# Optimization experiments

Hardware: AMD Instinct MI355X
Metric: run time of the kernel (lower is better)

Reference implementation:

```python
import jax, jax.numpy as jnp
import numpy as np

WS = (2, 7, 7)          # window size (s, h, w)
DIM = 192
HEADS = 6
HEAD_DIM = DIM // HEADS
N = WS[0] * WS[1] * WS[2]  # 98
TABLE = (2 * WS[0] - 1) * (2 * WS[1] - 1) * (2 * WS[2] - 1)  # 507


def _relative_position_index():
    coords = np.stack(np.meshgrid(np.arange(WS[0]), np.arange(WS[1]), np.arange(WS[2]), indexing='ij'))
    cf = coords.reshape(3, -1)                      # [3, N]
    rel = cf[:, :, None] - cf[:, None, :]           # [3, N, N]
    rel = rel.transpose(1, 2, 0).astype(np.int64)   # [N, N, 3]
    rel[..., 0] += WS[0] - 1
    rel[..., 1] += WS[1] - 1
    rel[..., 2] += WS[2] - 1
    rel[..., 0] *= 3 * WS[1] - 1  # faithful to source (quirky multiplier)
    rel[..., 1] *= 2 * WS[1] - 1
    return jnp.asarray(rel.sum(-1), dtype=jnp.int32)  # [N, N]


def setup_inputs() -> dict:
    key = jax.random.key(0)
    ks = jax.random.split(key, 8)
    B_ = 1024
    nW = 64
    skip = jax.random.normal(ks[0], (B_, N, DIM), dtype=jnp.float32)
    x_up = jax.random.normal(ks[1], (B_, N, DIM), dtype=jnp.float32)
    mask = jax.random.normal(ks[2], (nW, N, N), dtype=jnp.float32)
    kv_w = jax.random.normal(ks[3], (DIM, 2 * DIM), dtype=jnp.float32) * 0.02
    kv_b = jnp.zeros((2 * DIM,), dtype=jnp.float32)
    proj_w = jax.random.normal(ks[4], (DIM, DIM), dtype=jnp.float32) * 0.02
    proj_b = jnp.zeros((DIM,), dtype=jnp.float32)
    rpb_table = jax.random.normal(ks[5], (TABLE, HEADS), dtype=jnp.float32) * 0.02
    rel_idx = _relative_position_index()
    return {"skip": skip, "x_up": x_up, "mask": mask, "kv_w": kv_w, "kv_b": kv_b,
            "proj_w": proj_w, "proj_b": proj_b, "rpb_table": rpb_table, "rel_idx": rel_idx}


def reference(skip, x_up, mask, kv_w, kv_b, proj_w, proj_b, rpb_table, rel_idx):
    B_, n, C = skip.shape
    nW = mask.shape[0]
    scale = HEAD_DIM ** -0.5
    kv = skip @ kv_w + kv_b                                # [B_, N, 2C]
    kv = kv.reshape(B_, n, 2, HEADS, HEAD_DIM)
    k = kv[:, :, 0]                                        # [B_, N, H, hd]
    v = kv[:, :, 1]
    q = x_up.reshape(B_, n, HEADS, HEAD_DIM) * scale
    attn = jnp.einsum('bqhd,bkhd->bhqk', q, k)             # [B_, H, N, N]
    bias = rpb_table[rel_idx]                              # [N, N, H]
    attn = attn + jnp.transpose(bias, (2, 0, 1))[None]
    attn = attn.reshape(B_ // nW, nW, HEADS, n, n) + mask[None, :, None]
    attn = attn.reshape(B_, HEADS, n, n)
    attn = jax.nn.softmax(attn, axis=-1)
    out = jnp.einsum('bhqk,bkhd->bqhd', attn, v).reshape(B_, n, C)
    return out @ proj_w + proj_b
```

## Files before the change

### kernel.cpp

```cpp
#include <hip/hip_runtime.h>

#define NTOK 98
#define DIM 192
#define HEADS 6
#define SCALE 0.17677669529663687f

using shortx8 = __attribute__((ext_vector_type(8))) short;
using floatx4 = __attribute__((ext_vector_type(4))) float;

static __device__ __forceinline__ unsigned short f2bf(float f) {
    unsigned u = __float_as_uint(f);
    u += 0x7FFFu + ((u >> 16) & 1u);
    return (unsigned short)(u >> 16);
}

static __device__ __forceinline__ shortx8 pack8(const float* p, float scale) {
    float4 a = *(const float4*)p;
    float4 b = *(const float4*)(p + 4);
    shortx8 t;
    t[0] = (short)f2bf(a.x * scale); t[1] = (short)f2bf(a.y * scale);
    t[2] = (short)f2bf(a.z * scale); t[3] = (short)f2bf(a.w * scale);
    t[4] = (short)f2bf(b.x * scale); t[5] = (short)f2bf(b.y * scale);
    t[6] = (short)f2bf(b.z * scale); t[7] = (short)f2bf(b.w * scale);
    return t;
}

static __device__ __forceinline__ shortx8 frag_from_words(unsigned w0, unsigned w1,
                                                          unsigned w2, unsigned w3) {
    union { unsigned u[4]; shortx8 s; } t;
    t.u[0] = w0; t.u[1] = w1; t.u[2] = w2; t.u[3] = w3;
    return t.s;
}

template <bool HI>
static __device__ __forceinline__ shortx8 xchg4(unsigned lo0, unsigned lo1,
                                                unsigned hi0, unsigned hi1,
                                                int A0b, int A1b, bool hiSel) {
    unsigned l0 = (unsigned)__builtin_amdgcn_ds_bpermute(A0b, (int)lo0);
    unsigned l1 = (unsigned)__builtin_amdgcn_ds_bpermute(A0b, (int)lo1);
    unsigned l2 = (unsigned)__builtin_amdgcn_ds_bpermute(A1b, (int)lo0);
    unsigned l3 = (unsigned)__builtin_amdgcn_ds_bpermute(A1b, (int)lo1);
    unsigned h0 = 0, h1 = 0, h2 = 0, h3 = 0;
    if (HI) {
        h0 = (unsigned)__builtin_amdgcn_ds_bpermute(A0b, (int)hi0);
        h1 = (unsigned)__builtin_amdgcn_ds_bpermute(A0b, (int)hi1);
        h2 = (unsigned)__builtin_amdgcn_ds_bpermute(A1b, (int)hi0);
        h3 = (unsigned)__builtin_amdgcn_ds_bpermute(A1b, (int)hi1);
    }
    return frag_from_words(hiSel ? h0 : l0, hiSel ? h1 : l1,
                           hiSel ? h2 : l2, hiSel ? h3 : l3);
}

__global__ void prep_kernel(const float* __restrict__ rpb, const int* __restrict__ relidx,
                            const float* __restrict__ mask,
                            const float* __restrict__ kvw, const float* __restrict__ pw,
                            float* __restrict__ biasT, float* __restrict__ maskT,
                            unsigned short* __restrict__ kvB, unsigned short* __restrict__ pB) {
    int e = blockIdx.x * 256 + threadIdx.x;
    if (e < HEADS * NTOK * NTOK) {
        int h = e / (NTOK * NTOK), rem = e % (NTOK * NTOK);
        int j = rem / NTOK, i = rem % NTOK;
        biasT[e] = rpb[relidx[i * NTOK + j] * HEADS + h];
    }
    if (e < 64 * NTOK * NTOK) {
        int wd = e / (NTOK * NTOK), rem = e % (NTOK * NTOK);
        int j = rem / NTOK, i = rem % NTOK;
        maskT[e] = mask[((size_t)wd * NTOK + i) * NTOK + j];
    }
    if (e < 73728) {
        int jj = e & 7, lane = (e >> 3) & 63, t = e >> 9;
        int NT = t % 24, ks = t / 24;
        int c = ks * 32 + (lane >> 4) * 8 + jj;
        int n = NT * 16 + (lane & 15);
        kvB[e] = f2bf(kvw[c * 384 + n]);
    }
    if (e < 36864) {
        int jj = e & 7, lane = (e >> 3) & 63, t = e >> 9;
        int NT = t % 12, ks = t / 12;
        int c = ks * 32 + (lane >> 4) * 8 + jj;
        int n = NT * 16 + (lane & 15);
        pB[e] = f2bf(pw[c * 192 + n]);
    }
}

__global__ __launch_bounds__(448, 2) void attn_kernel(
    const float* __restrict__ skip, const float* __restrict__ xup,
    const float* __restrict__ kv_b,
    const float* __restrict__ biasT, const float* __restrict__ maskT,
    const unsigned short* __restrict__ kvB,
    float* __restrict__ out) {

    __shared__ __align__(16) unsigned short kB3[3 * 7 * 512];
    __shared__ __align__(16) unsigned short vB3[3 * 2 * 4 * 512];

    const int tid  = threadIdx.x;
    const int w    = tid >> 6;
    const int lane = tid & 63;
    const int l15  = lane & 15;
    const int quad = lane >> 4;
    const int win  = blockIdx.x >> 1;
    const int g    = blockIdx.x & 1;

    for (int e = tid; e < 6 * 512; e += 448)
        vB3[(e / 512) * 2048 + 3 * 512 + (e & 511)] = 0;
    __syncthreads();

    const int mA  = w * 16 + l15;
    const int mAc = mA < NTOK ? mA : 97;

    const int A0b = ((32 * (quad & 1) + l15) << 2);
    const int A1b = A0b + 64;

    {
        shortx8 afr[6];
        const float* sr = skip + ((size_t)win * NTOK + mAc) * DIM + quad * 8;
        #pragma unroll
        for (int ks = 0; ks < 6; ++ks) afr[ks] = pack8(sr + ks * 32, 1.0f);
        #pragma unroll
        for (int nt = 0; nt < 12; ++nt) {
            const int NTg = (nt < 6) ? (6 * g + nt) : (6 + 6 * g + nt);
            const float cb = kv_b[NTg * 16 + l15];
            floatx4 acc = {cb, cb, cb, cb};
            #pragma unroll
            for (int ks = 0; ks < 6; ++ks) {
                shortx8 bf = *(const shortx8*)(kvB + ((size_t)((ks * 24 + NTg) * 64 + lane)) * 8);
                acc = __builtin_amdgcn_mfma_f32_16x16x32_bf16(afr[ks], bf, acc, 0, 0, 0);
            }
            if (nt < 6) {
                const int ch = nt * 16 + l15, hh = ch >> 5, dh = ch & 31;
                const int base = ((hh * 7 + w) * 64) * 8 + (dh & 7);
                const int lphi = ((dh >> 3) & 3) << 4;
                #pragma unroll
                for (int r = 0; r < 4; ++r) {
                    int mm = quad * 4 + r;
                    kB3[base + (mm | lphi) * 8] = f2bf(acc[r]);
                }
            } else {
                const int cv = (nt - 6) * 16 + l15, hh = cv >> 5, dh = cv & 31, ntv = dh >> 4;
                #pragma unroll
                for (int r = 0; r < 4; ++r) {
                    int m = w * 16 + quad * 4 + r;
                    if (m < NTOK) {
                        int lp = (dh & 15) | (((m >> 3) & 3) << 4);
                        vB3[(((hh * 2 + ntv) * 4 + (m >> 5)) * 64 + lp) * 8 + (m & 7)] = f2bf(acc[r]);
                    }
                }
            }
        }
    }
    __syncthreads();

    #pragma unroll
    for (int hp = 0; hp < 3; ++hp) {
        const int h = 3 * g + hp;
        shortx8 qf = pack8(xup + ((size_t)win * NTOK + mAc) * DIM + h * 32 + quad * 8, SCALE);

        floatx4 S[7];
        {
            const float* bT = biasT + (size_t)h * (NTOK * NTOK);
            const float* mT = maskT + (size_t)(win & 63) * (NTOK * NTOK);
            #pragma unroll
            for (int nt = 0; nt < 7; ++nt) {
                #pragma unroll
                for (int r = 0; r < 4; ++r) {
                    int j = nt * 16 + quad * 4 + r;
                    S[nt][r] = (j < NTOK) ? (bT[j * NTOK + mAc] + mT[j * NTOK + mAc])
                                          : -1e30f;
                }
            }
        }
        #pragma unroll
        for (int nt = 0; nt < 7; ++nt) {
            shortx8 bk = *(const shortx8*)&kB3[((hp * 7 + nt) * 64 + lane) * 8];
            S[nt] = __builtin_amdgcn_mfma_f32_16x16x32_bf16(bk, qf, S[nt], 0, 0, 0);
        }
        float mx;
        {
            float m0 = fmaxf(fmaxf(S[0][0], S[0][1]), fmaxf(S[0][2], S[0][3]));
            float m1 = fmaxf(fmaxf(S[1][0], S[1][1]), fmaxf(S[1][2], S[1][3]));
            float m2 = fmaxf(fmaxf(S[2][0], S[2][1]), fmaxf(S[2][2], S[2][3]));
            float m3 = fmaxf(fmaxf(S[3][0], S[3][1]), fmaxf(S[3][2], S[3][3]));
            float m4 = fmaxf(fmaxf(S[4][0], S[4][1]), fmaxf(S[4][2], S[4][3]));
            float m5 = fmaxf(fmaxf(S[5][0], S[5][1]), fmaxf(S[5][2], S[5][3]));
            float m6 = fmaxf(fmaxf(S[6][0], S[6][1]), fmaxf(S[6][2], S[6][3]));
            mx = fmaxf(fmaxf(fmaxf(m0, m1), fmaxf(m2, m3)), fmaxf(fmaxf(m4, m5), m6));
            mx = fmaxf(mx, __shfl_xor(mx, 16));
            mx = fmaxf(mx, __shfl_xor(mx, 32));
        }
        float sm = 0.f;
        #pragma unroll
        for (int nt = 0; nt < 7; ++nt) {
            #pragma unroll
            for (int r = 0; r < 4; ++r) { S[nt][r] = __expf(S[nt][r] - mx); }
            sm += (S[nt][0] + S[nt][1]) + (S[nt][2] + S[nt][3]);
        }
        sm += __shfl_xor(sm, 16);
        sm += __shfl_xor(sm, 32);
        const float inv = 1.0f / sm;

        unsigned pk[7][2];
        #pragma unroll
        for (int nt = 0; nt < 7; ++nt) {
            pk[nt][0] = (unsigned)f2bf(S[nt][0]) | ((unsigned)f2bf(S[nt][1]) << 16);
            pk[nt][1] = (unsigned)f2bf(S[nt][2]) | ((unsigned)f2bf(S[nt][3]) << 16);
        }
        floatx4 o0 = {0.f, 0.f, 0.f, 0.f}, o1 = {0.f, 0.f, 0.f, 0.f};
        const bool hiSel = (quad & 2) != 0;
        #pragma unroll
        for (int ks = 0; ks < 4; ++ks) {
            shortx8 pfr;
            if (ks < 3)
                pfr = xchg4<true>(pk[2 * ks][0], pk[2 * ks][1],
                                  pk[2 * ks + 1][0], pk[2 * ks + 1][1], A0b, A1b, hiSel);
            else
                pfr = xchg4<false>(pk[6][0], pk[6][1], 0u, 0u, A0b, A1b, hiSel);
            shortx8 vb0 = *(const shortx8*)&vB3[(((hp * 2 + 0) * 4 + ks) * 64 + lane) * 8];
            o0 = __builtin_amdgcn_mfma_f32_16x16x32_bf16(vb0, pfr, o0, 0, 0, 0);
            shortx8 vb1 = *(const shortx8*)&vB3[(((hp * 2 + 1) * 4 + ks) * 64 + lane) * 8];
            o1 = __builtin_amdgcn_mfma_f32_16x16x32_bf16(vb1, pfr, o1, 0, 0, 0);
        }
        if (mA < NTOK) {
            float* orow = out + ((size_t)win * NTOK + mA) * DIM + h * 32;
            #pragma unroll
            for (int r = 0; r < 4; ++r) {
                orow[quad * 4 + r]      = o0[r] * inv;
                orow[16 + quad * 4 + r] = o1[r] * inv;
            }
        }
    }
}

__global__ __launch_bounds__(128, 8) void proj_kernel(
    float* __restrict__ io, const unsigned short* __restrict__ pB,
    const float* __restrict__ pb) {
    const int tid  = threadIdx.x;
    const int lane = tid & 63;
    const int l15  = lane & 15;
    const int quad = lane >> 4;
    const int idx  = blockIdx.x * 2 + (tid >> 6);
    const int win  = idx / 7;
    const int mt   = idx - win * 7;

    float* base = io + (size_t)win * NTOK * DIM;
    const int mA  = mt * 16 + l15;
    const int mAc = mA < NTOK ? mA : 97;

    shortx8 afr[6];
    {
        const float* ar = base + mAc * DIM + quad * 8;
        #pragma unroll
        for (int ks = 0; ks < 6; ++ks) afr[ks] = pack8(ar + ks * 32, 1.0f);
    }
    #pragma unroll
    for (int nt = 0; nt < 12; ++nt) {
        const int n = nt * 16 + l15;
        const float bb = pb[n];
        floatx4 acc = {bb, bb, bb, bb};
        #pragma unroll
        for (int ks = 0; ks < 6; ++ks) {
            shortx8 bf = *(const shortx8*)(pB + ((size_t)((ks * 12 + nt) * 64 + lane)) * 8);
            acc = __builtin_amdgcn_mfma_f32_16x16x32_bf16(afr[ks], bf, acc, 0, 0, 0);
        }
        #pragma unroll
        for (int r = 0; r < 4; ++r) {
            int m = mt * 16 + quad * 4 + r;
            if (m < NTOK) base[m * DIM + n] = acc[r];
        }
    }
}

extern "C" void kernel_launch(void* const* d_in, const int* in_sizes, int n_in,
                              void* d_out, int out_size, void* d_ws, size_t ws_size,
                              hipStream_t stream) {
    const float* skip   = (const float*)d_in[0];
    const float* x_up   = (const float*)d_in[1];
    const float* mask   = (const float*)d_in[2];
    const float* kv_w   = (const float*)d_in[3];
    const float* kv_b   = (const float*)d_in[4];
    const float* proj_w = (const float*)d_in[5];
    const float* proj_b = (const float*)d_in[6];
    const float* rpb    = (const float*)d_in[7];
    const int*   relidx = (const int*)d_in[8];
    float* out = (float*)d_out;

    float*          biasT = (float*)d_ws;
    float*          maskT = (float*)((char*)d_ws + 230496);
    unsigned short* kvB   = (unsigned short*)((char*)d_ws + 2689120);
    unsigned short* pB    = (unsigned short*)((char*)d_ws + 2836576);

    prep_kernel<<<2402, 256, 0, stream>>>(rpb, relidx, mask, kv_w, proj_w,
                                          biasT, maskT, kvB, pB);
    attn_kernel<<<2048, 448, 0, stream>>>(skip, x_up, kv_b, biasT, maskT, kvB, out);
    proj_kernel<<<3584, 128, 0, stream>>>(out, pB, proj_b);
}
```

Before: 362.3 us.

## Pad bias/mask rows for vector loads and pass bf16 MFMA fragments to projection

Bias and mask tables are re-laid out row-major with rows padded to 112 columns, using -1e30 and 0 as fill. This lets the attention kernel load them as float4 without bounds checks instead of doing strided scalar gathers. The attention kernel now writes its output as bf16, already packed in MFMA A-fragment order, into the output buffer. The projection kernel, one block per window with a barrier before overwriting in place, reads those fragments directly instead of reloading and converting fp32. This cuts global traffic for the intermediate, at the cost of extra scratch layout coupling and an in-place aliasing hazard guarded only within each block.

```diff
diff --git a/kernel.cpp b/kernel.cpp
--- a/kernel.cpp
+++ b/kernel.cpp
@@ -54,18 +54,18 @@
 __global__ void prep_kernel(const float* __restrict__ rpb, const int* __restrict__ relidx,
                             const float* __restrict__ mask,
                             const float* __restrict__ kvw, const float* __restrict__ pw,
-                            float* __restrict__ biasT, float* __restrict__ maskT,
+                            float* __restrict__ biasP, float* __restrict__ maskP,
                             unsigned short* __restrict__ kvB, unsigned short* __restrict__ pB) {
     int e = blockIdx.x * 256 + threadIdx.x;
-    if (e < HEADS * NTOK * NTOK) {
-        int h = e / (NTOK * NTOK), rem = e % (NTOK * NTOK);
-        int j = rem / NTOK, i = rem % NTOK;
-        biasT[e] = rpb[relidx[i * NTOK + j] * HEADS + h];
-    }
-    if (e < 64 * NTOK * NTOK) {
-        int wd = e / (NTOK * NTOK), rem = e % (NTOK * NTOK);
-        int j = rem / NTOK, i = rem % NTOK;
-        maskT[e] = mask[((size_t)wd * NTOK + i) * NTOK + j];
+    if (e < HEADS * NTOK * 112) {
+        int h = e / (NTOK * 112), rem = e % (NTOK * 112);
+        int i = rem / 112, j = rem % 112;
+        biasP[e] = (j < NTOK) ? rpb[relidx[i * NTOK + j] * HEADS + h] : -1e30f;
+    }
+    if (e < 64 * NTOK * 112) {
+        int wd = e / (NTOK * 112), rem = e % (NTOK * 112);
+        int i = rem / 112, j = rem % 112;
+        maskP[e] = (j < NTOK) ? mask[((size_t)wd * NTOK + i) * NTOK + j] : 0.f;
     }
     if (e < 73728) {
         int jj = e & 7, lane = (e >> 3) & 63, t = e >> 9;
@@ -86,9 +86,9 @@
 __global__ __launch_bounds__(448, 2) void attn_kernel(
     const float* __restrict__ skip, const float* __restrict__ xup,
     const float* __restrict__ kv_b,
-    const float* __restrict__ biasT, const float* __restrict__ maskT,
+    const float* __restrict__ biasP, const float* __restrict__ maskP,
     const unsigned short* __restrict__ kvB,
-    float* __restrict__ out) {
+    unsigned short* __restrict__ outS) {
 
     __shared__ __align__(16) unsigned short kB3[3 * 7 * 512];
     __shared__ __align__(16) unsigned short vB3[3 * 2 * 4 * 512];
@@ -157,16 +157,14 @@
 
         floatx4 S[7];
         {
-            const float* bT = biasT + (size_t)h * (NTOK * NTOK);
-            const float* mT = maskT + (size_t)(win & 63) * (NTOK * NTOK);
+            const float* bp = biasP + ((size_t)h * NTOK + mAc) * 112;
+            const float* mp = maskP + ((size_t)(win & 63) * NTOK + mAc) * 112;
             #pragma unroll
             for (int nt = 0; nt < 7; ++nt) {
-                #pragma unroll
-                for (int r = 0; r < 4; ++r) {
-                    int j = nt * 16 + quad * 4 + r;
-                    S[nt][r] = (j < NTOK) ? (bT[j * NTOK + mAc] + mT[j * NTOK + mAc])
-                                          : -1e30f;
-                }
+                float4 b4 = *(const float4*)(bp + nt * 16 + quad * 4);
+                float4 m4 = *(const float4*)(mp + nt * 16 + quad * 4);
+                S[nt][0] = b4.x + m4.x; S[nt][1] = b4.y + m4.y;
+                S[nt][2] = b4.z + m4.z; S[nt][3] = b4.w + m4.w;
             }
         }
         #pragma unroll
@@ -219,38 +217,33 @@
             shortx8 vb1 = *(const shortx8*)&vB3[(((hp * 2 + 1) * 4 + ks) * 64 + lane) * 8];
             o1 = __builtin_amdgcn_mfma_f32_16x16x32_bf16(vb1, pfr, o1, 0, 0, 0);
         }
-        if (mA < NTOK) {
-            float* orow = out + ((size_t)win * NTOK + mA) * DIM + h * 32;
-            #pragma unroll
-            for (int r = 0; r < 4; ++r) {
-                orow[quad * 4 + r]      = o0[r] * inv;
-                orow[16 + quad * 4 + r] = o1[r] * inv;
-            }
-        }
-    }
-}
-
-__global__ __launch_bounds__(128, 8) void proj_kernel(
+        unsigned w0 = (unsigned)f2bf(o0[0] * inv) | ((unsigned)f2bf(o0[1] * inv) << 16);
+        unsigned w1 = (unsigned)f2bf(o0[2] * inv) | ((unsigned)f2bf(o0[3] * inv) << 16);
+        unsigned w2 = (unsigned)f2bf(o1[0] * inv) | ((unsigned)f2bf(o1[1] * inv) << 16);
+        unsigned w3 = (unsigned)f2bf(o1[2] * inv) | ((unsigned)f2bf(o1[3] * inv) << 16);
+        shortx8 oa = xchg4<true>(w0, w1, w2, w3, A0b, A1b, hiSel);
+        *(shortx8*)(outS + (size_t)win * 37632 + w * 3072 + h * 512 + lane * 8) = oa;
+    }
+}
+
+__global__ __launch_bounds__(448, 4) void proj_kernel(
     float* __restrict__ io, const unsigned short* __restrict__ pB,
     const float* __restrict__ pb) {
     const int tid  = threadIdx.x;
+    const int w    = tid >> 6;
     const int lane = tid & 63;
     const int l15  = lane & 15;
     const int quad = lane >> 4;
-    const int idx  = blockIdx.x * 2 + (tid >> 6);
-    const int win  = idx / 7;
-    const int mt   = idx - win * 7;
+    const int win  = blockIdx.x;
+
+    const unsigned short* slab = (const unsigned short*)io + (size_t)win * 37632 + w * 3072;
+    shortx8 afr[6];
+    #pragma unroll
+    for (int ks = 0; ks < 6; ++ks)
+        afr[ks] = *(const shortx8*)(slab + ks * 512 + lane * 8);
+    __syncthreads();
 
     float* base = io + (size_t)win * NTOK * DIM;
-    const int mA  = mt * 16 + l15;
-    const int mAc = mA < NTOK ? mA : 97;
-
-    shortx8 afr[6];
-    {
-        const float* ar = base + mAc * DIM + quad * 8;
-        #pragma unroll
-        for (int ks = 0; ks < 6; ++ks) afr[ks] = pack8(ar + ks * 32, 1.0f);
-    }
     #pragma unroll
     for (int nt = 0; nt < 12; ++nt) {
         const int n = nt * 16 + l15;
@@ -263,7 +256,7 @@
         }
         #pragma unroll
         for (int r = 0; r < 4; ++r) {
-            int m = mt * 16 + quad * 4 + r;
+            int m = w * 16 + quad * 4 + r;
             if (m < NTOK) base[m * DIM + n] = acc[r];
         }
     }
@@ -283,13 +276,14 @@
     const int*   relidx = (const int*)d_in[8];
     float* out = (float*)d_out;
 
-    float*          biasT = (float*)d_ws;
-    float*          maskT = (float*)((char*)d_ws + 230496);
-    unsigned short* kvB   = (unsigned short*)((char*)d_ws + 2689120);
-    unsigned short* pB    = (unsigned short*)((char*)d_ws + 2836576);
-
-    prep_kernel<<<2402, 256, 0, stream>>>(rpb, relidx, mask, kv_w, proj_w,
-                                          biasT, maskT, kvB, pB);
-    attn_kernel<<<2048, 448, 0, stream>>>(skip, x_up, kv_b, biasT, maskT, kvB, out);
-    proj_kernel<<<3584, 128, 0, stream>>>(out, pB, proj_b);
-}
+    float*          biasP = (float*)d_ws;
+    float*          maskP = (float*)((char*)d_ws + 263424);
+    unsigned short* kvB   = (unsigned short*)((char*)d_ws + 3073280);
+    unsigned short* pB    = (unsigned short*)((char*)d_ws + 3220736);
+
+    prep_kernel<<<2744, 256, 0, stream>>>(rpb, relidx, mask, kv_w, proj_w,
+                                          biasP, maskP, kvB, pB);
+    attn_kernel<<<2048, 448, 0, stream>>>(skip, x_up, kv_b, biasP, maskP, kvB,
+                                          (unsigned short*)out);
+    proj_kernel<<<1024, 448, 0, stream>>>(out, pB, proj_b);
+}
```

After: 326.1 us. -10.0%, faster.
